# Kernel optimization log

Measured on AMD Instinct MI355X. Metric: run time of the kernel, lower is better.

The kernel has to match this reference:

```python
import jax, jax.numpy as jnp
import numpy as np

TEMP = 0.5
EPS_NORM = 1e-12  # F.normalize clamp eps
EPS_ROW = 1e-8


def _l2_normalize(x):
    n = jnp.sqrt(jnp.sum(x * x, axis=1, keepdims=True))
    return x / jnp.maximum(n, EPS_NORM)


def _sim(z1, z2):
    # exp(cosine_sim / T), [N, N]
    z1 = _l2_normalize(z1)
    z2 = _l2_normalize(z2)
    return jnp.exp(jnp.matmul(z1, z2.T) / TEMP)


def _loss_term(mat, pos):
    row = mat / (jnp.sum(mat, axis=1, keepdims=True) + EPS_ROW)
    return -jnp.mean(jnp.log(jnp.sum(row * pos, axis=-1)))


def setup_inputs() -> dict:
    key = jax.random.key(0)
    k1, k2, k3 = jax.random.split(key, 3)
    N, D = 8192, 64
    z_mp = jax.random.normal(k1, (N, D), dtype=jnp.float32)
    z_sc = jax.random.normal(k2, (N, D), dtype=jnp.float32)
    # sparse binary positive mask with guaranteed self-positives on diagonal
    pos = (jax.random.uniform(k3, (N, N)) < 0.005).astype(jnp.float32)
    pos = jnp.maximum(pos, jnp.eye(N, dtype=jnp.float32))
    return {"z_mp": z_mp, "z_sc": z_sc, "pos": pos}


def reference(z_mp, z_sc, pos):
    m_mp2sc = _sim(z_mp, z_sc)        # [N, N]
    m_sc2mp = m_mp2sc.T               # [N, N]
    m_mp2mp = _sim(z_mp, z_mp)        # [N, N]
    m_sc2sc = _sim(z_sc, z_sc)        # [N, N]
    loss = (_loss_term(m_mp2sc, pos)
            + _loss_term(m_sc2mp, pos)
            + _loss_term(m_mp2mp, pos)
            + _loss_term(m_sc2sc, pos))
    return loss
```

## Files before the change

### kernel.cpp

```cpp
#include <hip/hip_runtime.h>

#define N 8192
#define D 64
#define JSPLIT 16
#define JSTEPS (N / 64 / JSPLIT)

typedef unsigned short ushort_t;
typedef __attribute__((ext_vector_type(8))) short bf16x8;
typedef __attribute__((ext_vector_type(4))) float f32x4;

#define TWO_OVER_LN2 2.885390081777927f

__device__ inline ushort_t f32_to_bf16(float f) {
    union { float f; unsigned u; } c; c.f = f;
    unsigned r = (c.u + 0x7FFFu + ((c.u >> 16) & 1u)) >> 16;
    return (ushort_t)r;
}

__global__ void normalize_kernel(const float* __restrict__ z_mp,
                                 const float* __restrict__ z_sc,
                                 ushort_t* __restrict__ zn) {
    int lane = threadIdx.x & 63;
    int row  = blockIdx.x * 4 + (threadIdx.x >> 6);
    const float* src = (row < N) ? z_mp : z_sc;
    int srow = row & (N - 1);
    float x = src[srow * D + lane];
    float s = x * x;
    #pragma unroll
    for (int m = 32; m; m >>= 1) s += __shfl_xor(s, m, 64);
    float n = sqrtf(s);
    float scale = 1.0f / fmaxf(n, 1e-12f);
    zn[row * D + lane] = f32_to_bf16(x * scale);
}

__global__ __launch_bounds__(256, 3) void contrast_main(
        const ushort_t* __restrict__ zn,
        const float* __restrict__ pos,
        float* __restrict__ accum) {
    int lane   = threadIdx.x & 63;
    int w      = threadIdx.x >> 6;
    int a      = w >> 1, b = w & 1;
    int term   = (a == 0) ? (b == 0 ? 2 : 0) : (b == 0 ? 1 : 3);
    int rquart = lane >> 4;
    int lcol   = lane & 15;

    const ushort_t* Az = zn + a * (N * D);
    const ushort_t* Bz = zn + b * (N * D);

    int I0 = blockIdx.x * 64;
    int J0 = blockIdx.y * (N / JSPLIT);

    bf16x8 af[4][2];
    #pragma unroll
    for (int r = 0; r < 4; ++r)
        #pragma unroll
        for (int s = 0; s < 2; ++s)
            af[r][s] = *(const bf16x8*)(Az + (I0 + 16 * r + lcol) * D + s * 32 + rquart * 8);

    float rs_acc[4][4];
    float ps_acc[4][4];
    #pragma unroll
    for (int r = 0; r < 4; ++r)
        #pragma unroll
        for (int e = 0; e < 4; ++e) { rs_acc[r][e] = 0.0f; ps_acc[r][e] = 0.0f; }

    for (int jj = 0; jj < JSTEPS; ++jj) {
        int Jc = J0 + jj * 64;

        bf16x8 bf[4][2];
        #pragma unroll
        for (int c = 0; c < 4; ++c)
            #pragma unroll
            for (int s = 0; s < 2; ++s)
                bf[c][s] = *(const bf16x8*)(Bz + (Jc + 4 * lcol + c) * D + s * 32 + rquart * 8);

        const float* prow = pos + (long)(I0 + rquart * 4) * N + (Jc + 4 * lcol);

        f32x4 pv[2][4];
        #pragma unroll
        for (int e = 0; e < 4; ++e)
            pv[0][e] = *(const f32x4*)(prow + (long)e * N);

        #pragma unroll
        for (int r = 0; r < 4; ++r) {
            if (r < 3) {
                #pragma unroll
                for (int e = 0; e < 4; ++e)
                    pv[(r + 1) & 1][e] = *(const f32x4*)(prow + (long)(16 * (r + 1) + e) * N);
            }

            f32x4 acc[4];
            #pragma unroll
            for (int c = 0; c < 4; ++c) acc[c] = (f32x4){0.f, 0.f, 0.f, 0.f};
            #pragma unroll
            for (int s = 0; s < 2; ++s)
                #pragma unroll
                for (int c = 0; c < 4; ++c)
                    acc[c] = __builtin_amdgcn_mfma_f32_16x16x32_bf16(
                        af[r][s], bf[c][s], acc[c], 0, 0, 0);

            #pragma unroll
            for (int e = 0; e < 4; ++e) {
                f32x4 p = pv[r & 1][e];
                float rs = rs_acc[r][e], ps = ps_acc[r][e];
                #pragma unroll
                for (int c = 0; c < 4; ++c) {
                    float eV = exp2f(acc[c][e] * TWO_OVER_LN2);
                    rs += eV;
                    ps = fmaf(eV, p[c], ps);
                }
                rs_acc[r][e] = rs; ps_acc[r][e] = ps;
            }
        }
    }

    #pragma unroll
    for (int r = 0; r < 4; ++r)
        #pragma unroll
        for (int e = 0; e < 4; ++e) {
            float rs = rs_acc[r][e], ps = ps_acc[r][e];
            #pragma unroll
            for (int m = 1; m < 16; m <<= 1) {
                rs += __shfl_xor(rs, m, 64);
                ps += __shfl_xor(ps, m, 64);
            }
            rs_acc[r][e] = rs; ps_acc[r][e] = ps;
        }

    if (lcol == 0) {
        #pragma unroll
        for (int r = 0; r < 4; ++r)
            #pragma unroll
            for (int e = 0; e < 4; ++e) {
                int gi = I0 + 16 * r + rquart * 4 + e;
                atomicAdd(&accum[term * 2 * N + gi],     rs_acc[r][e]);
                atomicAdd(&accum[term * 2 * N + N + gi], ps_acc[r][e]);
            }
    }
}

__global__ void finalize_kernel(const float* __restrict__ accum,
                                float* __restrict__ out) {
    __shared__ float red[256];
    float local = 0.0f;
    for (int i = threadIdx.x; i < N; i += 256) {
        float s = 0.0f;
        #pragma unroll
        for (int t = 0; t < 4; ++t) {
            float rs = accum[t * 2 * N + i];
            float ps = accum[t * 2 * N + N + i];
            s += logf(ps / (rs + 1e-8f));
        }
        local += s;
    }
    red[threadIdx.x] = local;
    __syncthreads();
    for (int m = 128; m; m >>= 1) {
        if (threadIdx.x < m) red[threadIdx.x] += red[threadIdx.x + m];
        __syncthreads();
    }
    if (threadIdx.x == 0) out[0] = -red[0] / (float)N;
}

extern "C" void kernel_launch(void* const* d_in, const int* in_sizes, int n_in,
                              void* d_out, int out_size, void* d_ws, size_t ws_size,
                              hipStream_t stream) {
    const float* z_mp = (const float*)d_in[0];
    const float* z_sc = (const float*)d_in[1];
    const float* pos  = (const float*)d_in[2];
    float* out = (float*)d_out;

    ushort_t* zn = (ushort_t*)d_ws;
    float* accum = (float*)((char*)d_ws + (size_t)2 * N * D * sizeof(ushort_t));

    hipMemsetAsync(accum, 0, (size_t)4 * 2 * N * sizeof(float), stream);
    normalize_kernel<<<(2 * N) / 4, 256, 0, stream>>>(z_mp, z_sc, zn);
    dim3 grid(N / 64, JSPLIT);
    contrast_main<<<grid, 256, 0, stream>>>(zn, pos, accum);
    finalize_kernel<<<1, 256, 0, stream>>>(accum, out);
}
```

Baseline: 169.4 us.

## Share pos tiles via LDS with double-buffered async loads and prefetch B fragments

The positive-mask tile is now loaded once per block into double-buffered shared memory with global_load_lds, so the four waves share it instead of each loading pos separately. The next tile and the next B fragments are prefetched while the current step computes. The exp2 call uses the hardware builtin, and launch bounds drop from 3 to 2 blocks per CU to make room for the added registers and LDS. In exchange it adds a __syncthreads per step and lowers occupancy.

```diff
diff --git a/kernel.cpp b/kernel.cpp
--- a/kernel.cpp
+++ b/kernel.cpp
@@ -10,6 +10,15 @@
 typedef __attribute__((ext_vector_type(4))) float f32x4;
 
 #define TWO_OVER_LN2 2.885390081777927f
+
+#if __has_builtin(__builtin_amdgcn_exp2f)
+#define EXP2F(x) __builtin_amdgcn_exp2f(x)
+#else
+#define EXP2F(x) exp2f(x)
+#endif
+
+typedef __attribute__((address_space(1))) const unsigned int g_u32;
+typedef __attribute__((address_space(3))) unsigned int       l_u32;
 
 __device__ inline ushort_t f32_to_bf16(float f) {
     union { float f; unsigned u; } c; c.f = f;
@@ -33,16 +42,18 @@
     zn[row * D + lane] = f32_to_bf16(x * scale);
 }
 
-__global__ __launch_bounds__(256, 3) void contrast_main(
+__global__ __launch_bounds__(256, 2) void contrast_main(
         const ushort_t* __restrict__ zn,
         const float* __restrict__ pos,
         float* __restrict__ accum) {
-    int lane   = threadIdx.x & 63;
-    int w      = threadIdx.x >> 6;
-    int a      = w >> 1, b = w & 1;
-    int term   = (a == 0) ? (b == 0 ? 2 : 0) : (b == 0 ? 1 : 3);
-    int rquart = lane >> 4;
-    int lcol   = lane & 15;
+    __shared__ float ptile[2][64 * 64];
+
+    int lane = threadIdx.x & 63;
+    int w    = threadIdx.x >> 6;
+    int a = w >> 1, b = w & 1;
+    int term = (a == 0) ? (b == 0 ? 2 : 0) : (b == 0 ? 1 : 3);
+    int rq = lane >> 4;
+    int lc = lane & 15;
 
     const ushort_t* Az = zn + a * (N * D);
     const ushort_t* Bz = zn + b * (N * D);
@@ -55,40 +66,55 @@
     for (int r = 0; r < 4; ++r)
         #pragma unroll
         for (int s = 0; s < 2; ++s)
-            af[r][s] = *(const bf16x8*)(Az + (I0 + 16 * r + lcol) * D + s * 32 + rquart * 8);
-
-    float rs_acc[4][4];
-    float ps_acc[4][4];
+            af[r][s] = *(const bf16x8*)(Az + (I0 + 16 * r + lc) * D + s * 32 + rq * 8);
+
+    const ushort_t* bptr = Bz + ((size_t)(J0 + 4 * lc)) * D + rq * 8;
+    const float*    sptr = pos + (size_t)(I0 + w * 16 + rq) * N + J0 + lc * 4;
+
+    #define STAGE(bufv, jjv) do {                                              \
+        float* dbase_ = &ptile[bufv][w * 16 * 64];                             \
+        const float* sb_ = sptr + (size_t)(jjv) * 64;                          \
+        _Pragma("unroll")                                                      \
+        for (int it_ = 0; it_ < 4; ++it_) {                                    \
+            __builtin_amdgcn_global_load_lds(                                  \
+                (g_u32*)(sb_ + (size_t)it_ * 4 * N),                           \
+                (l_u32*)(dbase_ + it_ * 4 * 64), 16, 0, 0);                    \
+        }                                                                      \
+    } while (0)
+
+    bf16x8 bfc[4][2], bfn[4][2];
+
+    float rs_acc[4][4], ps_acc[4][4];
     #pragma unroll
     for (int r = 0; r < 4; ++r)
         #pragma unroll
         for (int e = 0; e < 4; ++e) { rs_acc[r][e] = 0.0f; ps_acc[r][e] = 0.0f; }
 
+    STAGE(0, 0);
+    #pragma unroll
+    for (int c = 0; c < 4; ++c)
+        #pragma unroll
+        for (int s = 0; s < 2; ++s)
+            bfc[c][s] = *(const bf16x8*)(bptr + c * D + s * 32);
+    __syncthreads();
+
+    #pragma unroll 2
     for (int jj = 0; jj < JSTEPS; ++jj) {
-        int Jc = J0 + jj * 64;
-
-        bf16x8 bf[4][2];
-        #pragma unroll
-        for (int c = 0; c < 4; ++c)
-            #pragma unroll
-            for (int s = 0; s < 2; ++s)
-                bf[c][s] = *(const bf16x8*)(Bz + (Jc + 4 * lcol + c) * D + s * 32 + rquart * 8);
-
-        const float* prow = pos + (long)(I0 + rquart * 4) * N + (Jc + 4 * lcol);
-
-        f32x4 pv[2][4];
-        #pragma unroll
-        for (int e = 0; e < 4; ++e)
-            pv[0][e] = *(const f32x4*)(prow + (long)e * N);
+        int buf = jj & 1;
+        if (jj + 1 < JSTEPS) {
+            STAGE(buf ^ 1, jj + 1);
+            const ushort_t* bn = bptr + 64 * D;
+            #pragma unroll
+            for (int c = 0; c < 4; ++c)
+                #pragma unroll
+                for (int s = 0; s < 2; ++s)
+                    bfn[c][s] = *(const bf16x8*)(bn + c * D + s * 32);
+        }
+
+        const float* tp = &ptile[buf][rq * 4 * 64 + lc * 4];
 
         #pragma unroll
         for (int r = 0; r < 4; ++r) {
-            if (r < 3) {
-                #pragma unroll
-                for (int e = 0; e < 4; ++e)
-                    pv[(r + 1) & 1][e] = *(const f32x4*)(prow + (long)(16 * (r + 1) + e) * N);
-            }
-
             f32x4 acc[4];
             #pragma unroll
             for (int c = 0; c < 4; ++c) acc[c] = (f32x4){0.f, 0.f, 0.f, 0.f};
@@ -97,22 +123,31 @@
                 #pragma unroll
                 for (int c = 0; c < 4; ++c)
                     acc[c] = __builtin_amdgcn_mfma_f32_16x16x32_bf16(
-                        af[r][s], bf[c][s], acc[c], 0, 0, 0);
+                        af[r][s], bfc[c][s], acc[c], 0, 0, 0);
 
             #pragma unroll
             for (int e = 0; e < 4; ++e) {
-                f32x4 p = pv[r & 1][e];
+                f32x4 p = *(const f32x4*)(tp + (16 * r + e) * 64);
                 float rs = rs_acc[r][e], ps = ps_acc[r][e];
                 #pragma unroll
                 for (int c = 0; c < 4; ++c) {
-                    float eV = exp2f(acc[c][e] * TWO_OVER_LN2);
+                    float eV = EXP2F(acc[c][e] * TWO_OVER_LN2);
                     rs += eV;
                     ps = fmaf(eV, p[c], ps);
                 }
                 rs_acc[r][e] = rs; ps_acc[r][e] = ps;
             }
         }
-    }
+
+        bptr += 64 * D;
+        #pragma unroll
+        for (int c = 0; c < 4; ++c)
+            #pragma unroll
+            for (int s = 0; s < 2; ++s)
+                bfc[c][s] = bfn[c][s];
+        __syncthreads();
+    }
+    #undef STAGE
 
     #pragma unroll
     for (int r = 0; r < 4; ++r)
@@ -127,12 +162,12 @@
             rs_acc[r][e] = rs; ps_acc[r][e] = ps;
         }
 
-    if (lcol == 0) {
+    if (lc == 0) {
         #pragma unroll
         for (int r = 0; r < 4; ++r)
             #pragma unroll
             for (int e = 0; e < 4; ++e) {
-                int gi = I0 + 16 * r + rquart * 4 + e;
+                int gi = I0 + 16 * r + rq * 4 + e;
                 atomicAdd(&accum[term * 2 * N + gi],     rs_acc[r][e]);
                 atomicAdd(&accum[term * 2 * N + N + gi], ps_acc[r][e]);
             }
```

After: 210.6 us. 1.24x slower.
